# Kernel tuning notes

Hardware: AMD Instinct MI355X
Metric: run time of the kernel (lower is better)

## Reference

```python
import jax, jax.numpy as jnp
import numpy as np
import math

B, N, M = 4, 512, 64
F, Q, H, R = 256, 16, 8, 32
D = F // H
ETA = 4.0
EPS = 1e-5
FFN_H = 512

def layer_norm(x, g, b):
    mu = jnp.mean(x, axis=-1, keepdims=True)
    var = jnp.mean((x - mu) ** 2, axis=-1, keepdims=True)
    return (x - mu) * jax.lax.rsqrt(var + EPS) * g + b

def setup_inputs() -> dict:
    key = jax.random.key(0)
    ks = jax.random.split(key, 24)
    def xav(k, shape):
        fan_in, fan_out = shape[1], shape[0]
        std = math.sqrt(2.0 / (fan_in + fan_out))
        return jax.random.normal(k, shape, dtype=jnp.float32) * std
    inp = {
        'a': jax.random.normal(ks[0], (B, N, F), dtype=jnp.float32),
        'charges': jax.random.normal(ks[1], (B, N, Q), dtype=jnp.float32),
        'idx_j': jax.random.randint(ks[2], (B, N, M), 0, N),
        'd_ij': jax.random.uniform(ks[3], (B, N, M), dtype=jnp.float32) * 5.0,
        'mask_ij': jax.random.bernoulli(ks[4], 0.3, (B, N, M)),
        'radial_shifts': jnp.linspace(0.5, 5.0, R, dtype=jnp.float32),
        'Wq': xav(ks[5], (F, F + Q)), 'bq': jnp.zeros((F,), jnp.float32),
        'Wk': xav(ks[6], (F, F + Q)), 'bk': jnp.zeros((F,), jnp.float32),
        'Wv': xav(ks[7], (F, F + Q)), 'bv': jnp.zeros((F,), jnp.float32),
        'Wrb': xav(ks[8], (H, R)), 'brb': jnp.zeros((H,), jnp.float32),
        'Wout': xav(ks[9], (F, 2 * F + R)), 'bout': jnp.zeros((F,), jnp.float32),
        'g1': jnp.ones((F,), jnp.float32), 'b1': jnp.zeros((F,), jnp.float32),
        'g2': jnp.ones((F,), jnp.float32), 'b2': jnp.zeros((F,), jnp.float32),
        'Wf1': xav(ks[10], (FFN_H, F)), 'bf1': jnp.zeros((FFN_H,), jnp.float32),
        'Wf2': xav(ks[11], (F, FFN_H)), 'bf2': jnp.zeros((F,), jnp.float32),
    }
    return inp

def reference(a, charges, idx_j, d_ij, mask_ij, radial_shifts,
              Wq, bq, Wk, bk, Wv, bv, Wrb, brb, Wout, bout,
              g1, b1, g2, b2, Wf1, bf1, Wf2, bf2):
    bidx = jnp.arange(B)[:, None, None]
    a_j = a[bidx, idx_j]          # [B,N,M,F]
    q_j = charges[bidx, idx_j]    # [B,N,M,Q]
    center = jnp.concatenate([a, charges], axis=-1)       # [B,N,F+Q]
    neigh = jnp.concatenate([a_j, q_j], axis=-1)          # [B,N,M,F+Q]
    q = (center @ Wq.T + bq).reshape(B, N, H, D)
    k = (neigh @ Wk.T + bk).reshape(B, N, M, H, D)
    v = (neigh @ Wv.T + bv).reshape(B, N, M, H, D)
    # radial basis: exp(-eta*(d - shift)^2)  -> [B,N,M,R]
    radial = jnp.exp(-ETA * (d_ij[..., None] - radial_shifts) ** 2)
    scores = jnp.einsum('bnhd,bnmhd->bnmh', q, k) / math.sqrt(D)
    scores = scores + radial @ Wrb.T + brb                # [B,N,M,H]
    scores = jnp.swapaxes(scores, -1, -2)                 # [B,N,H,M]
    scores = jnp.where(mask_ij[:, :, None, :], -jnp.inf, scores)
    attn = jax.nn.softmax(scores, axis=-1)
    attn = jnp.nan_to_num(attn, nan=0.0, posinf=0.0, neginf=0.0)
    context = jnp.einsum('bnhm,bnmhd->bnhd', attn, v).reshape(B, N, F)
    radial_context = jnp.einsum('bnhm,bnmg->bnhg', attn, radial).mean(axis=-2)  # [B,N,R]
    update = jnp.concatenate([a, context, radial_context], axis=-1) @ Wout.T + bout
    x = layer_norm(a + update, g1, b1)
    ff = jax.nn.gelu(x @ Wf1.T + bf1, approximate=False) @ Wf2.T + bf2
    return layer_norm(x + ff, g2, b2)
```

## Files before the change

### kernel.cpp

```cpp
#include <hip/hip_runtime.h>
#include <hip/hip_bf16.h>
#include <math.h>

#define Bb 4
#define Nn 512
#define Mm 64
#define Ff 256
#define Qq 16
#define Hh 8
#define Rr 32
#define FFNH 512
#define ROWS (Bb*Nn)
#define KIN (Ff+Qq)
#define KINP 288
#define KOUT (2*Ff+Rr)

typedef short short8 __attribute__((ext_vector_type(8)));
typedef unsigned short ushort8 __attribute__((ext_vector_type(8)));
typedef float f32x4 __attribute__((ext_vector_type(4)));

__device__ inline unsigned short f2b(float f) {
    union { float f; unsigned u; } c; c.f = f;
    unsigned r = c.u + 0x7fffu + ((c.u >> 16) & 1u);
    return (unsigned short)(r >> 16);
}
__device__ inline float b2f(unsigned short u) {
    union { unsigned u; float f; } c; c.u = ((unsigned)u) << 16;
    return c.f;
}

#define OFF_CENTER 0
#define OFF_WQKV   (OFF_CENTER + ROWS*KINP)
#define OFF_WOUT   (OFF_WQKV + 768*KINP)
#define OFF_WF1    (OFF_WOUT + Ff*KOUT)
#define OFF_WF2    (OFF_WF1 + FFNH*Ff)
#define OFF_U      (OFF_WF2 + Ff*FFNH)
#define OFF_XB     (OFF_U + ROWS*KOUT)
#define OFF_FFH    (OFF_XB + ROWS*Ff)
#define OFF_QKVB   (OFF_FFH + ROWS*FFNH)
#define CONV_TOTAL OFF_U
#define CONV_BLK   (CONV_TOTAL/256)
#define A2U_BLK    (ROWS*Ff/256)
#define MSK_BLK    (Bb*Nn*Mm/256)

__global__ __launch_bounds__(256) void prep(const float* __restrict__ a,
                                            const float* __restrict__ ch,
                                            const float* __restrict__ Wq,
                                            const float* __restrict__ Wk,
                                            const float* __restrict__ Wv,
                                            const float* __restrict__ Wout,
                                            const float* __restrict__ Wf1,
                                            const float* __restrict__ Wf2,
                                            const unsigned char* __restrict__ mask,
                                            int* __restrict__ flag,
                                            unsigned short* __restrict__ arena) {
    int bid = blockIdx.x, tid = threadIdx.x;
    if (bid < CONV_BLK) {
        int i = bid * 256 + tid;
        float v;
        if (i < OFF_WQKV) {
            int row = i / KINP, c = i - row * KINP;
            v = (c < Ff) ? a[(size_t)row * Ff + c] : (c < KIN ? ch[(size_t)row * Qq + (c - Ff)] : 0.f);
        } else if (i < OFF_WOUT) {
            int j = i - OFF_WQKV;
            int n = j / KINP, c = j - n * KINP;
            const float* W = n < 256 ? Wq : (n < 512 ? Wk : Wv);
            int nr = n & 255;
            v = (c < KIN) ? W[(size_t)nr * KIN + c] : 0.f;
        } else if (i < OFF_WF1) {
            v = Wout[i - OFF_WOUT];
        } else if (i < OFF_WF2) {
            v = Wf1[i - OFF_WF1];
        } else {
            v = Wf2[i - OFF_WF2];
        }
        arena[i] = f2b(v);
    } else if (bid < CONV_BLK + A2U_BLK) {
        int j = (bid - CONV_BLK) * 256 + tid;
        int row = j >> 8, col = j & 255;
        arena[OFF_U + (size_t)row * KOUT + col] = f2b(a[j]);
    } else {
        int i = (bid - CONV_BLK - A2U_BLK) * 256 + tid;
        if ((i & 3) && mask[i]) *flag = 1;
    }
}

template<int KT, int SPLIT, int MODE>
__global__ __launch_bounds__(256) void gemm_mfma(const unsigned short* __restrict__ Ab, int lda,
                                                 const unsigned short* __restrict__ Wb, int ldw,
                                                 const float* __restrict__ b0,
                                                 const float* __restrict__ b1,
                                                 const float* __restrict__ b2,
                                                 float* __restrict__ C,
                                                 unsigned short* __restrict__ Cb,
                                                 int ldc, size_t pstride) {
    __shared__ unsigned short As[2][64][32];
    __shared__ unsigned short Bs[2][64][32];
    int tid = threadIdx.x;
    int colbase = blockIdx.x * 64;
    int rowbase = blockIdx.y * 64;
    constexpr int TPER = (KT + SPLIT - 1) / SPLIT;
    int t0 = blockIdx.z * TPER;
    int NL = KT - t0; if (NL > TPER) NL = TPER;

    int sr = tid >> 2, sl = tid & 3;
    const unsigned short* Ap = Ab + (size_t)(rowbase + sr) * lda + sl * 8;
    const unsigned short* Wp = Wb + (size_t)(colbase + sr) * ldw + sl * 8;
    int ssw = (sl ^ (sr & 3)) * 8;

    int wave = tid >> 6, lane = tid & 63;
    int wr = (wave >> 1) * 32, wc = (wave & 1) * 32;
    int lrow = lane & 15;
    int kslot = lane >> 4;
    int sp = (kslot ^ (lane & 3)) * 8;

    uint4 av, wv;
    auto prefetch = [&](int t) {
        av = *reinterpret_cast<const uint4*>(Ap + (size_t)t * 32);
        wv = *reinterpret_cast<const uint4*>(Wp + (size_t)t * 32);
    };
    auto writeLDS = [&](int buf) {
        *reinterpret_cast<uint4*>(&As[buf][sr][ssw]) = av;
        *reinterpret_cast<uint4*>(&Bs[buf][sr][ssw]) = wv;
    };

    f32x4 acc[2][2] = {};
    prefetch(t0);
    writeLDS(0);
    __syncthreads();
    for (int tt = 0; tt < NL; ++tt) {
        if (tt + 1 < NL) prefetch(t0 + tt + 1);
        int buf = tt & 1;
        short8 a0 = *reinterpret_cast<const short8*>(&As[buf][wr + lrow][sp]);
        short8 a1 = *reinterpret_cast<const short8*>(&As[buf][wr + 16 + lrow][sp]);
        short8 bv0 = *reinterpret_cast<const short8*>(&Bs[buf][wc + lrow][sp]);
        short8 bv1 = *reinterpret_cast<const short8*>(&Bs[buf][wc + 16 + lrow][sp]);
        acc[0][0] = __builtin_amdgcn_mfma_f32_16x16x32_bf16(a0, bv0, acc[0][0], 0, 0, 0);
        acc[0][1] = __builtin_amdgcn_mfma_f32_16x16x32_bf16(a0, bv1, acc[0][1], 0, 0, 0);
        acc[1][0] = __builtin_amdgcn_mfma_f32_16x16x32_bf16(a1, bv0, acc[1][0], 0, 0, 0);
        acc[1][1] = __builtin_amdgcn_mfma_f32_16x16x32_bf16(a1, bv1, acc[1][1], 0, 0, 0);
        if (tt + 1 < NL) {
            writeLDS((tt + 1) & 1);
            __syncthreads();
        }
    }

    const float* bias = b0;
    if (MODE == 1) {
        int sel = colbase >> 8;
        bias = sel == 0 ? b0 : (sel == 1 ? b1 : b2);
    }
    int colq = (colbase & 255);
    float* Cp = (MODE == 0) ? C + (size_t)blockIdx.z * pstride : C;
    #pragma unroll
    for (int fr = 0; fr < 2; ++fr) {
        #pragma unroll
        for (int fc = 0; fc < 2; ++fc) {
            int coll = wc + fc * 16 + (lane & 15);
            int col = colbase + coll;
            #pragma unroll
            for (int i = 0; i < 4; ++i) {
                int row = rowbase + wr + fr * 16 + (lane >> 4) * 4 + i;
                float v = acc[fr][fc][i];
                if (MODE == 0) {
                    Cp[(size_t)row * ldc + col] = v;
                } else if (MODE == 1) {
                    Cb[(size_t)row * ldc + col] = f2b(v + bias[colq + coll]);
                } else {
                    v += bias[col];
                    v = 0.5f * v * (1.0f + erff(v * 0.70710678118654752f));
                    Cb[(size_t)row * ldc + col] = f2b(v);
                }
            }
        }
    }
}

__global__ __launch_bounds__(256) void attn_kernel(const unsigned short* __restrict__ QKV,
                                                   const int* __restrict__ idx_j,
                                                   const float* __restrict__ d_ij,
                                                   const void* __restrict__ mask,
                                                   const float* __restrict__ shifts,
                                                   const float* __restrict__ Wrb,
                                                   const float* __restrict__ brb,
                                                   const int* __restrict__ flag,
                                                   unsigned short* __restrict__ Ub) {
    __shared__ unsigned short Kt[2][16][280];
    __shared__ float rad[Mm][36];
    __shared__ float att[Hh][Mm];
    __shared__ float attbar[Mm];
    __shared__ int   jl[Mm];
    __shared__ float dv[Mm];
    __shared__ int   maskf[Mm];
    __shared__ float shs[Rr];

    int row = blockIdx.x;
    int b = row >> 9;
    int tid = threadIdx.x;
    bool boolmask = (*flag != 0);

    if (tid < Mm) jl[tid] = idx_j[row * Mm + tid];
    else if (tid < 128) { int m = tid - 64; dv[m] = d_ij[row * Mm + m]; }
    else if (tid < 160) shs[tid - 128] = shifts[tid - 128];
    else if (tid >= 192) {
        int m = tid - 192;
        maskf[m] = boolmask ? (int)((const unsigned char*)mask)[row * Mm + m]
                            : ((const int*)mask)[row * Mm + m];
    }

    int half = tid & 1;
    int p = tid >> 1;
    int hh = p >> 4;
    int ml = p & 15;
    float qf[16];
    {
        const unsigned short* qrow = QKV + (size_t)row * 768 + hh * 32 + half * 16;
        ushort8 q0 = *reinterpret_cast<const ushort8*>(qrow);
        ushort8 q1 = *reinterpret_cast<const ushort8*>(qrow + 8);
        #pragma unroll
        for (int i = 0; i < 8; ++i) { qf[i] = b2f(q0[i]); qf[8 + i] = b2f(q1[i]); }
    }
    float4 wreg[4];
    #pragma unroll
    for (int c = 0; c < 4; ++c)
        wreg[c] = *reinterpret_cast<const float4*>(Wrb + hh * Rr + half * 16 + c * 4);
    float brbh = brb[hh];
    __syncthreads();

    auto stage = [&](int t, int seg, int buf) {
        #pragma unroll
        for (int q = 0; q < 2; ++q) {
            int chunk = q * 256 + tid;
            int r = chunk >> 5, s = chunk & 31;
            int j = jl[t * 16 + r];
            const uint4* src = reinterpret_cast<const uint4*>(QKV + (size_t)(b * Nn + j) * 768 + seg);
            uint4 v = src[s];
            *reinterpret_cast<uint4*>(&Kt[buf][r][s * 8]) = v;
        }
    };

    #pragma unroll
    for (int it = 0; it < 8; ++it) {
        int i = tid + it * 256;
        int m = i >> 5, r = i & 31;
        float t = dv[m] - shs[r];
        rad[m][r] = expf(-4.0f * t * t);
    }
    stage(0, 256, 0);
    __syncthreads();

    for (int t = 0; t < 4; ++t) {
        if (t < 3) stage(t + 1, 256, (t + 1) & 1);
        int buf = t & 1;
        const unsigned short* kr = &Kt[buf][ml][hh * 32 + half * 16];
        ushort8 k0 = *reinterpret_cast<const ushort8*>(kr);
        ushort8 k1 = *reinterpret_cast<const ushort8*>(kr + 8);
        float accK = 0.f;
        #pragma unroll
        for (int i = 0; i < 8; ++i) accK = fmaf(qf[i], b2f(k0[i]), accK);
        #pragma unroll
        for (int i = 0; i < 8; ++i) accK = fmaf(qf[8 + i], b2f(k1[i]), accK);
        float accR = 0.f;
        #pragma unroll
        for (int c = 0; c < 4; ++c) {
            float4 rv = *reinterpret_cast<const float4*>(&rad[t * 16 + ml][half * 16 + c * 4]);
            accR += wreg[c].x * rv.x + wreg[c].y * rv.y + wreg[c].z * rv.z + wreg[c].w * rv.w;
        }
        float tv = accK * 0.17677669529663687f + accR;
        tv += __shfl_xor(tv, 1);
        if (!half) {
            int m = t * 16 + ml;
            att[hh][m] = maskf[m] ? -INFINITY : (tv + brbh);
        }
        __syncthreads();
    }

    {
        int h = tid >> 5, l = tid & 31;
        float s0 = att[h][l], s1 = att[h][l + 32];
        float mx = fmaxf(s0, s1);
        #pragma unroll
        for (int off = 16; off; off >>= 1) mx = fmaxf(mx, __shfl_xor(mx, off, 32));
        float e0 = 0.f, e1 = 0.f;
        if (mx != -INFINITY) {
            e0 = expf(s0 - mx);
            e1 = expf(s1 - mx);
        }
        float sm = e0 + e1;
        #pragma unroll
        for (int off = 16; off; off >>= 1) sm += __shfl_xor(sm, off, 32);
        float inv = sm > 0.f ? 1.f / sm : 0.f;
        att[h][l] = e0 * inv;
        att[h][l + 32] = e1 * inv;
    }
    stage(0, 512, 0);
    __syncthreads();

    float ctx = 0.f;
    int h2 = tid >> 5, d0 = tid & 31;
    for (int t = 0; t < 4; ++t) {
        if (t < 3) stage(t + 1, 512, (t + 1) & 1);
        int buf = t & 1;
        #pragma unroll
        for (int m = 0; m < 16; ++m)
            ctx = fmaf(att[h2][t * 16 + m], b2f(Kt[buf][m][h2 * 32 + d0]), ctx);
        if (t == 0 && tid < Mm) {
            float sv = 0.f;
            #pragma unroll
            for (int h = 0; h < Hh; ++h) sv += att[h][tid];
            attbar[tid] = sv * 0.125f;
        }
        __syncthreads();
    }

    Ub[(size_t)row * KOUT + Ff + tid] = f2b(ctx);

    if (tid < 64) {
        int g = tid >> 1;
        float acc = 0.f;
        #pragma unroll
        for (int i = 0; i < 32; ++i) {
            int m = half * 32 + i;
            acc = fmaf(attbar[m], rad[m][g], acc);
        }
        acc += __shfl_xor(acc, 1);
        if (!half) Ub[(size_t)row * KOUT + 2 * Ff + g] = f2b(acc);
    }
}

template<int S, int WB>
__global__ __launch_bounds__(256) void add_ln_c(const float* __restrict__ x0,
                                                const float* __restrict__ part, size_t pstride,
                                                const float* __restrict__ bias,
                                                const float* __restrict__ g,
                                                const float* __restrict__ be,
                                                float* __restrict__ outp,
                                                unsigned short* __restrict__ xb) {
    int tid = threadIdx.x;
    int wave = tid >> 6, lane = tid & 63;
    int row = blockIdx.x * 4 + wave;
    size_t off = (size_t)row * Ff + lane * 4;
    float4 v = *reinterpret_cast<const float4*>(x0 + off);
    float4 bb = *reinterpret_cast<const float4*>(bias + lane * 4);
    v.x += bb.x; v.y += bb.y; v.z += bb.z; v.w += bb.w;
    #pragma unroll
    for (int s = 0; s < S; ++s) {
        float4 p = *reinterpret_cast<const float4*>(part + (size_t)s * pstride + off);
        v.x += p.x; v.y += p.y; v.z += p.z; v.w += p.w;
    }
    float sm = v.x + v.y + v.z + v.w;
    #pragma unroll
    for (int o = 32; o; o >>= 1) sm += __shfl_xor(sm, o, 64);
    float mu = sm * (1.f / Ff);
    float4 c = {v.x - mu, v.y - mu, v.z - mu, v.w - mu};
    float s2 = c.x * c.x + c.y * c.y + c.z * c.z + c.w * c.w;
    #pragma unroll
    for (int o = 32; o; o >>= 1) s2 += __shfl_xor(s2, o, 64);
    float inv = rsqrtf(s2 * (1.f / Ff) + 1e-5f);
    float4 gg = *reinterpret_cast<const float4*>(g + lane * 4);
    float4 ee = *reinterpret_cast<const float4*>(be + lane * 4);
    float4 r;
    r.x = c.x * inv * gg.x + ee.x;
    r.y = c.y * inv * gg.y + ee.y;
    r.z = c.z * inv * gg.z + ee.z;
    r.w = c.w * inv * gg.w + ee.w;
    *reinterpret_cast<float4*>(outp + off) = r;
    if (WB) {
        ushort4 u;
        u.x = f2b(r.x); u.y = f2b(r.y); u.z = f2b(r.z); u.w = f2b(r.w);
        *reinterpret_cast<ushort4*>(&xb[off]) = u;
    }
}

extern "C" void kernel_launch(void* const* d_in, const int* in_sizes, int n_in,
                              void* d_out, int out_size, void* d_ws, size_t ws_size,
                              hipStream_t stream) {
    const float* a       = (const float*)d_in[0];
    const float* charges = (const float*)d_in[1];
    const int*   idx_j   = (const int*)  d_in[2];
    const float* d_ij    = (const float*)d_in[3];
    const void*  mask    =               d_in[4];
    const float* shifts  = (const float*)d_in[5];
    const float* Wq   = (const float*)d_in[6];  const float* bq   = (const float*)d_in[7];
    const float* Wk   = (const float*)d_in[8];  const float* bk   = (const float*)d_in[9];
    const float* Wv   = (const float*)d_in[10]; const float* bv   = (const float*)d_in[11];
    const float* Wrb  = (const float*)d_in[12]; const float* brb  = (const float*)d_in[13];
    const float* Wout = (const float*)d_in[14]; const float* bout = (const float*)d_in[15];
    const float* g1   = (const float*)d_in[16]; const float* b1   = (const float*)d_in[17];
    const float* g2   = (const float*)d_in[18]; const float* b2   = (const float*)d_in[19];
    const float* Wf1  = (const float*)d_in[20]; const float* bf1  = (const float*)d_in[21];
    const float* Wf2  = (const float*)d_in[22]; const float* bf2  = (const float*)d_in[23];
    float* outp = (float*)d_out;

    float* ws   = (float*)d_ws;
    int*   flag = (int*)d_ws;
    float* part = ws + 1024;
    float* xbuf = part + 1048576;
    unsigned short* arena = (unsigned short*)(xbuf + 524288);
    unsigned short* centerb = arena + OFF_CENTER;
    unsigned short* Wqkvb   = arena + OFF_WQKV;
    unsigned short* Woutb   = arena + OFF_WOUT;
    unsigned short* Wf1b    = arena + OFF_WF1;
    unsigned short* Wf2b    = arena + OFF_WF2;
    unsigned short* Ub      = arena + OFF_U;
    unsigned short* xb      = arena + OFF_XB;
    unsigned short* ffhb    = arena + OFF_FFH;
    unsigned short* QKVB16  = arena + OFF_QKVB;

    hipMemsetAsync(flag, 0, sizeof(int), stream);
    prep<<<CONV_BLK + A2U_BLK + MSK_BLK, 256, 0, stream>>>(
        a, charges, Wq, Wk, Wv, Wout, Wf1, Wf2, (const unsigned char*)mask, flag, arena);

    gemm_mfma<9, 1, 1><<<dim3(12, 32, 1), 256, 0, stream>>>(
        centerb, KINP, Wqkvb, KINP, bq, bk, bv, nullptr, QKVB16, 768, 0);

    attn_kernel<<<ROWS, 256, 0, stream>>>(QKVB16, idx_j, d_ij, mask, shifts, Wrb, brb, flag, Ub);

    gemm_mfma<17, 2, 0><<<dim3(4, 32, 2), 256, 0, stream>>>(
        Ub, KOUT, Woutb, KOUT, nullptr, nullptr, nullptr, part, nullptr, Ff, (size_t)ROWS * Ff);
    add_ln_c<2, 1><<<ROWS / 4, 256, 0, stream>>>(a, part, (size_t)ROWS * Ff, bout, g1, b1, xbuf, xb);

    gemm_mfma<8, 1, 2><<<dim3(8, 32, 1), 256, 0, stream>>>(
        xb, Ff, Wf1b, Ff, bf1, nullptr, nullptr, nullptr, ffhb, FFNH, 0);

    gemm_mfma<16, 2, 0><<<dim3(4, 32, 2), 256, 0, stream>>>(
        ffhb, FFNH, Wf2b, FFNH, nullptr, nullptr, nullptr, part, nullptr, Ff, (size_t)ROWS * Ff);
    add_ln_c<2, 0><<<ROWS / 4, 256, 0, stream>>>(xbuf, part, (size_t)ROWS * Ff, bf2, g2, b2, outp, nullptr);
}
```

Before: 65.64 us.

## Fuse fp32-to-bf16 conversion into GEMM loads and drop prep kernel and memset

Removes the separate prep kernel and the flag memset. Weights and activations are now converted from fp32 to bf16 inside each GEMM's global-load path, and the QKV GEMM reads a and charges directly. The mask-flag scan becomes an extra column of blocks in the QKV kernel, writing one flag per block row that the attention kernel ORs with a wave vote. Copying a into U moves into the attention kernel. This saves launches and a full round trip of converted data through memory, but every GEMM block now re-reads and re-converts fp32 weights, which doubles weight load bytes.

```diff
diff --git a/kernel.cpp b/kernel.cpp
--- a/kernel.cpp
+++ b/kernel.cpp
@@ -28,69 +28,128 @@
     union { unsigned u; float f; } c; c.u = ((unsigned)u) << 16;
     return c.f;
 }
-
-#define OFF_CENTER 0
-#define OFF_WQKV   (OFF_CENTER + ROWS*KINP)
-#define OFF_WOUT   (OFF_WQKV + 768*KINP)
-#define OFF_WF1    (OFF_WOUT + Ff*KOUT)
-#define OFF_WF2    (OFF_WF1 + FFNH*Ff)
-#define OFF_U      (OFF_WF2 + Ff*FFNH)
-#define OFF_XB     (OFF_U + ROWS*KOUT)
-#define OFF_FFH    (OFF_XB + ROWS*Ff)
-#define OFF_QKVB   (OFF_FFH + ROWS*FFNH)
-#define CONV_TOTAL OFF_U
-#define CONV_BLK   (CONV_TOTAL/256)
-#define A2U_BLK    (ROWS*Ff/256)
-#define MSK_BLK    (Bb*Nn*Mm/256)
-
-__global__ __launch_bounds__(256) void prep(const float* __restrict__ a,
-                                            const float* __restrict__ ch,
-                                            const float* __restrict__ Wq,
-                                            const float* __restrict__ Wk,
-                                            const float* __restrict__ Wv,
-                                            const float* __restrict__ Wout,
-                                            const float* __restrict__ Wf1,
-                                            const float* __restrict__ Wf2,
-                                            const unsigned char* __restrict__ mask,
-                                            int* __restrict__ flag,
-                                            unsigned short* __restrict__ arena) {
-    int bid = blockIdx.x, tid = threadIdx.x;
-    if (bid < CONV_BLK) {
-        int i = bid * 256 + tid;
-        float v;
-        if (i < OFF_WQKV) {
-            int row = i / KINP, c = i - row * KINP;
-            v = (c < Ff) ? a[(size_t)row * Ff + c] : (c < KIN ? ch[(size_t)row * Qq + (c - Ff)] : 0.f);
-        } else if (i < OFF_WOUT) {
-            int j = i - OFF_WQKV;
-            int n = j / KINP, c = j - n * KINP;
-            const float* W = n < 256 ? Wq : (n < 512 ? Wk : Wv);
-            int nr = n & 255;
-            v = (c < KIN) ? W[(size_t)nr * KIN + c] : 0.f;
-        } else if (i < OFF_WF1) {
-            v = Wout[i - OFF_WOUT];
-        } else if (i < OFF_WF2) {
-            v = Wf1[i - OFF_WF1];
-        } else {
-            v = Wf2[i - OFF_WF2];
-        }
-        arena[i] = f2b(v);
-    } else if (bid < CONV_BLK + A2U_BLK) {
-        int j = (bid - CONV_BLK) * 256 + tid;
-        int row = j >> 8, col = j & 255;
-        arena[OFF_U + (size_t)row * KOUT + col] = f2b(a[j]);
-    } else {
-        int i = (bid - CONV_BLK - A2U_BLK) * 256 + tid;
-        if ((i & 3) && mask[i]) *flag = 1;
+__device__ inline uint4 pack8(float4 lo, float4 hi) {
+    uint4 u;
+    u.x = (unsigned)f2b(lo.x) | ((unsigned)f2b(lo.y) << 16);
+    u.y = (unsigned)f2b(lo.z) | ((unsigned)f2b(lo.w) << 16);
+    u.z = (unsigned)f2b(hi.x) | ((unsigned)f2b(hi.y) << 16);
+    u.w = (unsigned)f2b(hi.z) | ((unsigned)f2b(hi.w) << 16);
+    return u;
+}
+
+#define OFF_U     0
+#define OFF_XB    (OFF_U + ROWS*KOUT)
+#define OFF_FFH   (OFF_XB + ROWS*Ff)
+#define OFF_QKVB  (OFF_FFH + ROWS*FFNH)
+
+__global__ __launch_bounds__(256) void qkv_conv(const float* __restrict__ a,
+                                                const float* __restrict__ ch,
+                                                const float* __restrict__ Wq,
+                                                const float* __restrict__ Wk,
+                                                const float* __restrict__ Wv,
+                                                const float* __restrict__ bq,
+                                                const float* __restrict__ bk,
+                                                const float* __restrict__ bv,
+                                                const unsigned char* __restrict__ mask,
+                                                int* __restrict__ flagArr,
+                                                unsigned short* __restrict__ QKVb) {
+    int tid = threadIdx.x;
+    if (blockIdx.x == 12) {
+        __shared__ int bf_;
+        if (tid == 0) bf_ = 0;
+        __syncthreads();
+        int idx = blockIdx.y * 256 + tid;
+        uint4 v = reinterpret_cast<const uint4*>(mask)[idx];
+        unsigned m = (v.x | v.y | v.z | v.w) & 0xFFFFFF00u;
+        if (m) atomicOr(&bf_, 1);
+        __syncthreads();
+        if (tid == 0) flagArr[blockIdx.y] = bf_;
+        return;
+    }
+
+    __shared__ unsigned short As[2][64][32];
+    __shared__ unsigned short Bs[2][64][32];
+    int colbase = blockIdx.x * 64;
+    int rowbase = blockIdx.y * 64;
+
+    int sr = tid >> 2, sl = tid & 3;
+    int ssw = (sl ^ (sr & 3)) * 8;
+    int sel = colbase >> 8;
+    const float* Wsel = sel == 0 ? Wq : (sel == 1 ? Wk : Wv);
+    const float* bias = sel == 0 ? bq : (sel == 1 ? bk : bv);
+    int wrow = (colbase & 255) + sr;
+    int arow = rowbase + sr;
+
+    int wave = tid >> 6, lane = tid & 63;
+    int wr = (wave >> 1) * 32, wc = (wave & 1) * 32;
+    int lrow = lane & 15;
+    int kslot = lane >> 4;
+    int sp = (kslot ^ (lane & 3)) * 8;
+
+    uint4 av, wv;
+    auto prefetch = [&](int t) {
+        int gc = t * 32 + sl * 8;
+        float4 f0 = {0.f, 0.f, 0.f, 0.f}, f1 = f0, w0 = f0, w1 = f0;
+        if (gc < Ff) {
+            f0 = *reinterpret_cast<const float4*>(a + (size_t)arow * Ff + gc);
+            f1 = *reinterpret_cast<const float4*>(a + (size_t)arow * Ff + gc + 4);
+        } else if (gc < KIN) {
+            f0 = *reinterpret_cast<const float4*>(ch + (size_t)arow * Qq + (gc - Ff));
+            f1 = *reinterpret_cast<const float4*>(ch + (size_t)arow * Qq + (gc - Ff) + 4);
+        }
+        if (gc < KIN) {
+            w0 = *reinterpret_cast<const float4*>(Wsel + (size_t)wrow * KIN + gc);
+            w1 = *reinterpret_cast<const float4*>(Wsel + (size_t)wrow * KIN + gc + 4);
+        }
+        av = pack8(f0, f1);
+        wv = pack8(w0, w1);
+    };
+    auto writeLDS = [&](int buf) {
+        *reinterpret_cast<uint4*>(&As[buf][sr][ssw]) = av;
+        *reinterpret_cast<uint4*>(&Bs[buf][sr][ssw]) = wv;
+    };
+
+    f32x4 acc[2][2] = {};
+    prefetch(0);
+    writeLDS(0);
+    __syncthreads();
+    for (int tt = 0; tt < 9; ++tt) {
+        if (tt + 1 < 9) prefetch(tt + 1);
+        int buf = tt & 1;
+        short8 a0 = *reinterpret_cast<const short8*>(&As[buf][wr + lrow][sp]);
+        short8 a1 = *reinterpret_cast<const short8*>(&As[buf][wr + 16 + lrow][sp]);
+        short8 bv0 = *reinterpret_cast<const short8*>(&Bs[buf][wc + lrow][sp]);
+        short8 bv1 = *reinterpret_cast<const short8*>(&Bs[buf][wc + 16 + lrow][sp]);
+        acc[0][0] = __builtin_amdgcn_mfma_f32_16x16x32_bf16(a0, bv0, acc[0][0], 0, 0, 0);
+        acc[0][1] = __builtin_amdgcn_mfma_f32_16x16x32_bf16(a0, bv1, acc[0][1], 0, 0, 0);
+        acc[1][0] = __builtin_amdgcn_mfma_f32_16x16x32_bf16(a1, bv0, acc[1][0], 0, 0, 0);
+        acc[1][1] = __builtin_amdgcn_mfma_f32_16x16x32_bf16(a1, bv1, acc[1][1], 0, 0, 0);
+        if (tt + 1 < 9) {
+            writeLDS((tt + 1) & 1);
+            __syncthreads();
+        }
+    }
+
+    int colq = (colbase & 255);
+    #pragma unroll
+    for (int fr = 0; fr < 2; ++fr) {
+        #pragma unroll
+        for (int fc = 0; fc < 2; ++fc) {
+            int coll = wc + fc * 16 + (lane & 15);
+            int col = colbase + coll;
+            #pragma unroll
+            for (int i = 0; i < 4; ++i) {
+                int row = rowbase + wr + fr * 16 + (lane >> 4) * 4 + i;
+                QKVb[(size_t)row * 768 + col] = f2b(acc[fr][fc][i] + bias[colq + coll]);
+            }
+        }
     }
 }
 
 template<int KT, int SPLIT, int MODE>
-__global__ __launch_bounds__(256) void gemm_mfma(const unsigned short* __restrict__ Ab, int lda,
-                                                 const unsigned short* __restrict__ Wb, int ldw,
+__global__ __launch_bounds__(256) void gemm_wf32(const unsigned short* __restrict__ Ab, int lda,
+                                                 const float* __restrict__ Wf, int ldw,
                                                  const float* __restrict__ b0,
-                                                 const float* __restrict__ b1,
-                                                 const float* __restrict__ b2,
                                                  float* __restrict__ C,
                                                  unsigned short* __restrict__ Cb,
                                                  int ldc, size_t pstride) {
@@ -105,7 +164,7 @@
 
     int sr = tid >> 2, sl = tid & 3;
     const unsigned short* Ap = Ab + (size_t)(rowbase + sr) * lda + sl * 8;
-    const unsigned short* Wp = Wb + (size_t)(colbase + sr) * ldw + sl * 8;
+    const float* Wp = Wf + (size_t)(colbase + sr) * ldw + sl * 8;
     int ssw = (sl ^ (sr & 3)) * 8;
 
     int wave = tid >> 6, lane = tid & 63;
@@ -117,7 +176,9 @@
     uint4 av, wv;
     auto prefetch = [&](int t) {
         av = *reinterpret_cast<const uint4*>(Ap + (size_t)t * 32);
-        wv = *reinterpret_cast<const uint4*>(Wp + (size_t)t * 32);
+        float4 w0 = *reinterpret_cast<const float4*>(Wp + (size_t)t * 32);
+        float4 w1 = *reinterpret_cast<const float4*>(Wp + (size_t)t * 32 + 4);
+        wv = pack8(w0, w1);
     };
     auto writeLDS = [&](int buf) {
         *reinterpret_cast<uint4*>(&As[buf][sr][ssw]) = av;
@@ -145,29 +206,20 @@
         }
     }
 
-    const float* bias = b0;
-    if (MODE == 1) {
-        int sel = colbase >> 8;
-        bias = sel == 0 ? b0 : (sel == 1 ? b1 : b2);
-    }
-    int colq = (colbase & 255);
     float* Cp = (MODE == 0) ? C + (size_t)blockIdx.z * pstride : C;
     #pragma unroll
     for (int fr = 0; fr < 2; ++fr) {
         #pragma unroll
         for (int fc = 0; fc < 2; ++fc) {
-            int coll = wc + fc * 16 + (lane & 15);
-            int col = colbase + coll;
+            int col = colbase + wc + fc * 16 + (lane & 15);
             #pragma unroll
             for (int i = 0; i < 4; ++i) {
                 int row = rowbase + wr + fr * 16 + (lane >> 4) * 4 + i;
                 float v = acc[fr][fc][i];
                 if (MODE == 0) {
                     Cp[(size_t)row * ldc + col] = v;
-                } else if (MODE == 1) {
-                    Cb[(size_t)row * ldc + col] = f2b(v + bias[colq + coll]);
                 } else {
-                    v += bias[col];
+                    v += b0[col];
                     v = 0.5f * v * (1.0f + erff(v * 0.70710678118654752f));
                     Cb[(size_t)row * ldc + col] = f2b(v);
                 }
@@ -177,13 +229,14 @@
 }
 
 __global__ __launch_bounds__(256) void attn_kernel(const unsigned short* __restrict__ QKV,
+                                                   const float* __restrict__ a,
                                                    const int* __restrict__ idx_j,
                                                    const float* __restrict__ d_ij,
                                                    const void* __restrict__ mask,
                                                    const float* __restrict__ shifts,
                                                    const float* __restrict__ Wrb,
                                                    const float* __restrict__ brb,
-                                                   const int* __restrict__ flag,
+                                                   const int* __restrict__ flagArr,
                                                    unsigned short* __restrict__ Ub) {
     __shared__ unsigned short Kt[2][16][280];
     __shared__ float rad[Mm][36];
@@ -197,7 +250,7 @@
     int row = blockIdx.x;
     int b = row >> 9;
     int tid = threadIdx.x;
-    bool boolmask = (*flag != 0);
+    bool boolmask = __any(flagArr[tid & 31] != 0);
 
     if (tid < Mm) jl[tid] = idx_j[row * Mm + tid];
     else if (tid < 128) { int m = tid - 64; dv[m] = d_ij[row * Mm + m]; }
@@ -313,6 +366,7 @@
         __syncthreads();
     }
 
+    Ub[(size_t)row * KOUT + tid] = f2b(a[(size_t)row * Ff + tid]);
     Ub[(size_t)row * KOUT + Ff + tid] = f2b(ctx);
 
     if (tid < 64) {
@@ -392,38 +446,29 @@
     const float* Wf2  = (const float*)d_in[22]; const float* bf2  = (const float*)d_in[23];
     float* outp = (float*)d_out;
 
-    float* ws   = (float*)d_ws;
-    int*   flag = (int*)d_ws;
+    float* ws     = (float*)d_ws;
+    int*   flagArr = (int*)d_ws;
     float* part = ws + 1024;
     float* xbuf = part + 1048576;
     unsigned short* arena = (unsigned short*)(xbuf + 524288);
-    unsigned short* centerb = arena + OFF_CENTER;
-    unsigned short* Wqkvb   = arena + OFF_WQKV;
-    unsigned short* Woutb   = arena + OFF_WOUT;
-    unsigned short* Wf1b    = arena + OFF_WF1;
-    unsigned short* Wf2b    = arena + OFF_WF2;
-    unsigned short* Ub      = arena + OFF_U;
-    unsigned short* xb      = arena + OFF_XB;
-    unsigned short* ffhb    = arena + OFF_FFH;
-    unsigned short* QKVB16  = arena + OFF_QKVB;
-
-    hipMemsetAsync(flag, 0, sizeof(int), stream);
-    prep<<<CONV_BLK + A2U_BLK + MSK_BLK, 256, 0, stream>>>(
-        a, charges, Wq, Wk, Wv, Wout, Wf1, Wf2, (const unsigned char*)mask, flag, arena);
-
-    gemm_mfma<9, 1, 1><<<dim3(12, 32, 1), 256, 0, stream>>>(
-        centerb, KINP, Wqkvb, KINP, bq, bk, bv, nullptr, QKVB16, 768, 0);
-
-    attn_kernel<<<ROWS, 256, 0, stream>>>(QKVB16, idx_j, d_ij, mask, shifts, Wrb, brb, flag, Ub);
-
-    gemm_mfma<17, 2, 0><<<dim3(4, 32, 2), 256, 0, stream>>>(
-        Ub, KOUT, Woutb, KOUT, nullptr, nullptr, nullptr, part, nullptr, Ff, (size_t)ROWS * Ff);
+    unsigned short* Ub     = arena + OFF_U;
+    unsigned short* xb     = arena + OFF_XB;
+    unsigned short* ffhb   = arena + OFF_FFH;
+    unsigned short* QKVB16 = arena + OFF_QKVB;
+
+    qkv_conv<<<dim3(13, 32), 256, 0, stream>>>(
+        a, charges, Wq, Wk, Wv, bq, bk, bv, (const unsigned char*)mask, flagArr, QKVB16);
+
+    attn_kernel<<<ROWS, 256, 0, stream>>>(QKVB16, a, idx_j, d_ij, mask, shifts, Wrb, brb, flagArr, Ub);
+
+    gemm_wf32<17, 2, 0><<<dim3(4, 32, 2), 256, 0, stream>>>(
+        Ub, KOUT, Wout, KOUT, nullptr, part, nullptr, Ff, (size_t)ROWS * Ff);
     add_ln_c<2, 1><<<ROWS / 4, 256, 0, stream>>>(a, part, (size_t)ROWS * Ff, bout, g1, b1, xbuf, xb);
 
-    gemm_mfma<8, 1, 2><<<dim3(8, 32, 1), 256, 0, stream>>>(
-        xb, Ff, Wf1b, Ff, bf1, nullptr, nullptr, nullptr, ffhb, FFNH, 0);
-
-    gemm_mfma<16, 2, 0><<<dim3(4, 32, 2), 256, 0, stream>>>(
-        ffhb, FFNH, Wf2b, FFNH, nullptr, nullptr, nullptr, part, nullptr, Ff, (size_t)ROWS * Ff);
+    gemm_wf32<8, 1, 2><<<dim3(8, 32, 1), 256, 0, stream>>>(
+        xb, Ff, Wf1, Ff, bf1, nullptr, ffhb, FFNH, 0);
+
+    gemm_wf32<16, 2, 0><<<dim3(4, 32, 2), 256, 0, stream>>>(
+        ffhb, FFNH, Wf2, FFNH, nullptr, part, nullptr, Ff, (size_t)ROWS * Ff);
     add_ln_c<2, 0><<<ROWS / 4, 256, 0, stream>>>(xbuf, part, (size_t)ROWS * Ff, bf2, g2, b2, outp, nullptr);
 }
```

Result: no change. 65.66 us (+0.0%).
